# Optimization experiments

Measured on AMD Instinct MI355X. Metric: run time of the kernel, lower is better.

## Reference

```python
import jax, jax.numpy as jnp
import numpy as np

THRESHOLD = 0.5
NEG_POS_RATIO = 3
ALPHA = 1.0
B, P, C, O = 128, 8732, 21, 32


def xy_to_cxcy(xy):
    return jnp.concatenate([(xy[..., 2:] + xy[..., :2]) / 2, xy[..., 2:] - xy[..., :2]], axis=-1)


def cxcy_to_xy(cxcy):
    return jnp.concatenate([cxcy[..., :2] - cxcy[..., 2:] / 2, cxcy[..., :2] + cxcy[..., 2:] / 2], axis=-1)


def cxcy_to_gcxgcy(cxcy, priors_cxcy):
    g_cxcy = (cxcy[..., :2] - priors_cxcy[..., :2]) / (priors_cxcy[..., 2:] / 10.0)
    g_wh = jnp.log(cxcy[..., 2:] / priors_cxcy[..., 2:]) * 5.0
    return jnp.concatenate([g_cxcy, g_wh], axis=-1)


def find_jaccard_overlap(set1, set2):
    # set1: [O,4] xy, set2: [P,4] xy -> [O,P]
    lo = jnp.maximum(set1[:, None, :2], set2[None, :, :2])
    hi = jnp.minimum(set1[:, None, 2:], set2[None, :, 2:])
    inter = jnp.prod(jnp.clip(hi - lo, 0.0), axis=-1)
    a1 = jnp.prod(set1[:, 2:] - set1[:, :2], axis=-1)
    a2 = jnp.prod(set2[:, 2:] - set2[:, :2], axis=-1)
    union = a1[:, None] + a2[None, :] - inter
    return inter / union


def setup_inputs() -> dict:
    key = jax.random.key(0)
    k0, k1, k2, k3, k4, k5, k6 = jax.random.split(key, 7)
    predicted_locs = jax.random.normal(k0, (B, P, 4), jnp.float32)
    predicted_scores = jax.random.normal(k1, (B, P, C), jnp.float32)
    centers = jax.random.uniform(k2, (B, O, 2), jnp.float32, 0.2, 0.8)
    sizes = jax.random.uniform(k3, (B, O, 2), jnp.float32, 0.05, 0.3)
    boxes = jnp.concatenate([centers - sizes / 2, centers + sizes / 2], axis=-1)
    labels = jax.random.randint(k4, (B, O), 0, C)
    p_c = jax.random.uniform(k5, (P, 2), jnp.float32, 0.05, 0.95)
    p_wh = jax.random.uniform(k6, (P, 2), jnp.float32, 0.05, 0.5)
    priors_cxcy = jnp.concatenate([p_c, p_wh], axis=-1)
    return {"predicted_locs": predicted_locs, "predicted_scores": predicted_scores,
            "boxes": boxes, "labels": labels, "priors_cxcy": priors_cxcy}


def reference(predicted_locs, predicted_scores, boxes, labels, priors_cxcy):
    priors_xy = cxcy_to_xy(priors_cxcy)

    def match_one(boxes_i, labels_i):
        overlap = find_jaccard_overlap(boxes_i, priors_xy)           # [O,P]
        overlap_for_each_prior = jnp.max(overlap, axis=0)            # [P]
        object_for_each_prior = jnp.argmax(overlap, axis=0)          # [P]
        prior_for_each_object = jnp.argmax(overlap, axis=1)          # [O]
        object_for_each_prior = object_for_each_prior.at[prior_for_each_object].set(jnp.arange(O))
        overlap_for_each_prior = overlap_for_each_prior.at[prior_for_each_object].set(1.0)
        label_for_each_prior = labels_i[object_for_each_prior]
        label_for_each_prior = jnp.where(overlap_for_each_prior < THRESHOLD, 0, label_for_each_prior)
        true_locs_i = cxcy_to_gcxgcy(xy_to_cxcy(boxes_i[object_for_each_prior]), priors_cxcy)
        return label_for_each_prior, true_locs_i

    true_classes, true_locs = jax.vmap(match_one)(boxes, labels)     # [B,P], [B,P,4]

    positive = true_classes != 0                                     # [B,P]
    n_positives = jnp.sum(positive, axis=1)                          # [B]
    n_pos_total = jnp.sum(n_positives)

    # L1Loss (mean over selected positive elements, 4 per prior)
    abs_diff = jnp.abs(predicted_locs - true_locs)                   # [B,P,4]
    loc_loss = jnp.sum(abs_diff * positive[..., None]) / (n_pos_total.astype(jnp.float32) * 4.0)

    # per-element cross-entropy
    log_p = jax.nn.log_softmax(predicted_scores, axis=-1)            # [B,P,C]
    conf_loss_all = -jnp.take_along_axis(log_p, true_classes[..., None], axis=-1)[..., 0]  # [B,P]

    conf_loss_pos_sum = jnp.sum(jnp.where(positive, conf_loss_all, 0.0))
    conf_loss_neg = jnp.where(positive, 0.0, conf_loss_all)
    conf_loss_neg_sorted = -jnp.sort(-conf_loss_neg, axis=1)         # descending
    n_hard = NEG_POS_RATIO * n_positives                             # [B]
    hard_mask = jnp.arange(P)[None, :] < n_hard[:, None]             # [B,P]
    conf_loss_hard_neg_sum = jnp.sum(jnp.where(hard_mask, conf_loss_neg_sorted, 0.0))

    conf_loss = (conf_loss_hard_neg_sum + conf_loss_pos_sum) / n_pos_total.astype(jnp.float32)
    return conf_loss + ALPHA * loc_loss
```

## Files before the change

kernel.cpp:

```cpp
#include <hip/hip_runtime.h>
#include <hip/hip_bf16.h>

#define NB 128
#define NP 8732
#define NO 32
#define NC 21


__global__ __launch_bounds__(256) void k_init(int* ws) {
    int i = blockIdx.x * 256 + threadIdx.x;
    const int n = 36608 / 4;
    if (i < n) ws[i] = 0;
}

__device__ __forceinline__ float wave64_max_dpp(float m) {
    int v;
    v = __builtin_amdgcn_update_dpp(__float_as_int(m), __float_as_int(m), 0x111, 0xf, 0xf, false);
    m = fmaxf(m, __int_as_float(v));
    v = __builtin_amdgcn_update_dpp(__float_as_int(m), __float_as_int(m), 0x112, 0xf, 0xf, false);
    m = fmaxf(m, __int_as_float(v));
    v = __builtin_amdgcn_update_dpp(__float_as_int(m), __float_as_int(m), 0x114, 0xf, 0xf, false);
    m = fmaxf(m, __int_as_float(v));
    v = __builtin_amdgcn_update_dpp(__float_as_int(m), __float_as_int(m), 0x118, 0xf, 0xf, false);
    m = fmaxf(m, __int_as_float(v));
    v = __builtin_amdgcn_update_dpp(__float_as_int(m), __float_as_int(m), 0x142, 0xf, 0xf, false);
    m = fmaxf(m, __int_as_float(v));
    v = __builtin_amdgcn_update_dpp(__float_as_int(m), __float_as_int(m), 0x143, 0xf, 0xf, false);
    m = fmaxf(m, __int_as_float(v));
    return __int_as_float(__builtin_amdgcn_readlane(__float_as_int(m), 63));
}

__global__ __launch_bounds__(256) void k_match(const float* __restrict__ boxes,
                                               const float* __restrict__ priors,
                                               int* __restrict__ code,
                                               unsigned long long* __restrict__ packed) {
    int b = blockIdx.y;
    int tid = threadIdx.x;
    int base = blockIdx.x * 1024 + tid;
    int lane = tid & 63;

    __shared__ float4 sbox[NO];
    if (tid < NO)
        sbox[tid] = ((const float4*)(boxes + (size_t)b * NO * 4))[tid];
    __syncthreads();

    float px1[4], py1[4], px2[4], py2[4], pa[4];
    float bestv[4];
    int   besto[4];
#pragma unroll
    for (int j = 0; j < 4; ++j) {
        int p = base + 256 * j;
        int pp = p < NP ? p : NP - 1;
        float4 pr = ((const float4*)priors)[pp];
        px1[j] = pr.x - pr.z * 0.5f; py1[j] = pr.y - pr.w * 0.5f;
        px2[j] = pr.x + pr.z * 0.5f; py2[j] = pr.y + pr.w * 0.5f;
        pa[j]  = (px2[j] - px1[j]) * (py2[j] - py1[j]);
        bestv[j] = -1.0f; besto[j] = 0;
    }

    int wavep0 = blockIdx.x * 1024 + (tid & ~63);

#pragma unroll 2
    for (int o = 0; o < NO; ++o) {
        float4 bx = sbox[o];
        float a1 = (bx.z - bx.x) * (bx.w - bx.y);
        float iou[4];
#pragma unroll
        for (int j = 0; j < 4; ++j) {
            float lx = fmaxf(bx.x, px1[j]), ly = fmaxf(bx.y, py1[j]);
            float hx = fminf(bx.z, px2[j]), hy = fminf(bx.w, py2[j]);
            float iw = fmaxf(hx - lx, 0.0f), ih = fmaxf(hy - ly, 0.0f);
            float inter = iw * ih;
            iou[j] = inter / (a1 + pa[j] - inter);
            if (iou[j] > bestv[j]) { bestv[j] = iou[j]; besto[j] = o; }
        }
        float m = wave64_max_dpp(fmaxf(fmaxf(iou[0], iou[1]), fmaxf(iou[2], iou[3])));
        unsigned long long b0 = __ballot(iou[0] == m);
        unsigned long long b1 = __ballot(iou[1] == m);
        unsigned long long b2 = __ballot(iou[2] == m);
        unsigned long long b3 = __ballot(iou[3] == m);
        if (lane == 0) {
            unsigned long long bb; int jj;
            if (b0)      { bb = b0; jj = 0; }
            else if (b1) { bb = b1; jj = 1; }
            else if (b2) { bb = b2; jj = 2; }
            else         { bb = b3; jj = 3; }
            unsigned p = (unsigned)(wavep0 + 256 * jj) + (unsigned)(__ffsll(bb) - 1);
            unsigned long long key =
                ((unsigned long long)__float_as_uint(m) << 32) |
                (unsigned long long)(0xFFFFFFFFu - p);
            atomicMax(&packed[b * NO + o], key);
        }
    }
#pragma unroll
    for (int j = 0; j < 4; ++j) {
        int p = base + 256 * j;
        if (p < NP)
            code[(size_t)b * NP + p] = besto[j] | (bestv[j] >= 0.5f ? 256 : 0);
    }
}

__global__ __launch_bounds__(256) void k_loss(const float* __restrict__ plocs,
                                              const float* __restrict__ scores,
                                              const float* __restrict__ boxes,
                                              const int* __restrict__ labels,
                                              const float* __restrict__ priors,
                                              const int* __restrict__ code,
                                              const unsigned long long* __restrict__ packed,
                                              float* __restrict__ confneg,
                                              int* __restrict__ npos,
                                              double* __restrict__ accb) {
    __shared__ float srow[256 * NC];
    __shared__ unsigned spfl[NO];
    int b = blockIdx.y;
    int p0 = blockIdx.x * 256;
    int cnt = NP - p0; if (cnt > 256) cnt = 256;
    int nf4 = cnt * NC / 4;
    const float4* src4 = (const float4*)(scores + ((size_t)b * NP + p0) * NC);
    for (int i = threadIdx.x; i < nf4; i += 256)
        ((float4*)srow)[i] = src4[i];
    if (threadIdx.x < NO) {
        unsigned long long pk = packed[b * NO + threadIdx.x];
        spfl[threadIdx.x] = 0xFFFFFFFFu - (unsigned)(pk & 0xFFFFFFFFull);
    }
    __syncthreads();

    int p = p0 + threadIdx.x;
    float posconf = 0.0f, locpart = 0.0f;
    int isp = 0;

    if (p < NP) {
        int cd = code[(size_t)b * NP + p];
        int obj = cd & 255;
        int mat = cd >> 8;
#pragma unroll
        for (int o = 0; o < NO; ++o)
            if (spfl[o] == (unsigned)p) { obj = o; mat = 1; }
        int lbl = mat ? labels[b * NO + obj] : 0;

        const float* s = srow + threadIdx.x * NC;
        float m = s[0];
#pragma unroll
        for (int c = 1; c < NC; ++c) m = fmaxf(m, s[c]);
        float sum = 0.0f;
#pragma unroll
        for (int c = 0; c < NC; ++c) sum += __expf(s[c] - m);
        float conf = m + __logf(sum) - s[lbl];

        if (lbl != 0) {
            isp = 1;
            posconf = conf;
            float4 bx = ((const float4*)boxes)[b * NO + obj];
            float4 pr = ((const float4*)priors)[p];
            float cx = (bx.x + bx.z) * 0.5f, cy = (bx.y + bx.w) * 0.5f;
            float w = bx.z - bx.x, h = bx.w - bx.y;
            float gx = (cx - pr.x) / (pr.z * 0.1f);
            float gy = (cy - pr.y) / (pr.w * 0.1f);
            float gw = __logf(w / pr.z) * 5.0f;
            float gh = __logf(h / pr.w) * 5.0f;
            float4 pl = ((const float4*)plocs)[(size_t)b * NP + p];
            locpart = fabsf(pl.x - gx) + fabsf(pl.y - gy) +
                      fabsf(pl.z - gw) + fabsf(pl.w - gh);
        }
        confneg[(size_t)b * NP + p] = isp ? 0.0f : conf;
    }

    for (int s = 32; s > 0; s >>= 1) {
        posconf += __shfl_xor(posconf, s, 64);
        locpart += __shfl_xor(locpart, s, 64);
        isp     += __shfl_xor(isp, s, 64);
    }
    __shared__ float w0[4], w1[4];
    __shared__ int wc[4];
    int wid = threadIdx.x >> 6, lane = threadIdx.x & 63;
    if (lane == 0) { w0[wid] = posconf; w1[wid] = locpart; wc[wid] = isp; }
    __syncthreads();
    if (threadIdx.x == 0) {
        float t0 = w0[0] + w0[1] + w0[2] + w0[3];
        float t1 = w1[0] + w1[1] + w1[2] + w1[3];
        int   tc = wc[0] + wc[1] + wc[2] + wc[3];
        atomicAdd(&npos[b], tc);
        atomicAdd(&accb[b * 3 + 0], (double)t0);
        atomicAdd(&accb[b * 3 + 1], (double)t1);
    }
}

__global__ __launch_bounds__(1024) void k_topk(const float* __restrict__ confneg,
                                               const int* __restrict__ npos,
                                               double* __restrict__ accb,
                                               int* __restrict__ donecnt,
                                               float* __restrict__ out) {
    __shared__ int   si2[2][16];
    __shared__ int   si[16];
    __shared__ double sd[16];
    int tid = threadIdx.x, b = blockIdx.x;
    int lane = tid & 63, wid = tid >> 6;

    const float* src = confneg + (size_t)b * NP;
    float val[9];
#pragma unroll
    for (int j = 0; j < 9; ++j) {
        int i = tid + j * 1024;
        val[j] = (i < NP) ? src[i] : 0.0f;
    }
    int k = npos[b] * 3;
    if (k > NP) k = NP;

    if (k > 0) {
        unsigned T = 0;
        int par = 0;
        for (int bit = 30; bit >= 0; --bit) {
            unsigned cand = T | (1u << bit);
            int cnt = 0;
#pragma unroll
            for (int j = 0; j < 9; ++j)
                cnt += __popcll(__ballot(__float_as_uint(val[j]) >= cand));
            if (lane == 0) si2[par][wid] = cnt;
            __syncthreads();
            int t = 0;
#pragma unroll
            for (int w = 0; w < 16; ++w) t += si2[par][w];
            par ^= 1;
            if (t >= k) T = cand;
        }

        int cgt = 0;
        double sgt = 0.0;
#pragma unroll
        for (int j = 0; j < 9; ++j) {
            unsigned u = __float_as_uint(val[j]);
            if (u > T) { cgt++; sgt += (double)val[j]; }
        }
        for (int s = 32; s > 0; s >>= 1) {
            cgt += __shfl_xor(cgt, s, 64);
            sgt += __shfl_xor(sgt, s, 64);
        }
        if (lane == 0) { si[wid] = cgt; sd[wid] = sgt; }
        __syncthreads();
        if (tid == 0) {
            int cg = 0; double sg = 0.0;
            for (int w = 0; w < 16; ++w) { cg += si[w]; sg += sd[w]; }
            accb[b * 3 + 2] = sg + (double)(k - cg) * (double)__uint_as_float(T);
        }
    }

    __shared__ int samlast;
    if (tid == 0) {
        __threadfence();
        int prev = atomicAdd(donecnt, 1);
        samlast = (prev == NB - 1) ? 1 : 0;
    }
    __syncthreads();
    if (!samlast) return;
    __threadfence();

    double pc = 0.0, lc = 0.0, hn = 0.0, np_ = 0.0;
    if (tid < NB) {
        pc  = accb[tid * 3 + 0];
        lc  = accb[tid * 3 + 1];
        hn  = atomicAdd(&accb[tid * 3 + 2], 0.0);
        np_ = (double)npos[tid];
    }
    if (tid < 128) {
        for (int s = 32; s > 0; s >>= 1) {
            pc  += __shfl_xor(pc, s, 64);
            lc  += __shfl_xor(lc, s, 64);
            hn  += __shfl_xor(hn, s, 64);
            np_ += __shfl_xor(np_, s, 64);
        }
        if (lane == 0) { sd[wid * 4 + 0] = pc; sd[wid * 4 + 1] = lc;
                         sd[wid * 4 + 2] = hn; sd[wid * 4 + 3] = np_; }
    }
    __syncthreads();
    if (tid == 0) {
        double P = sd[0] + sd[4];
        double L = sd[1] + sd[5];
        double H = sd[2] + sd[6];
        double nt = sd[3] + sd[7];
        out[0] = (float)((H + P) / nt + L / (nt * 4.0));
    }
}

extern "C" void kernel_launch(void* const* d_in, const int* in_sizes, int n_in,
                              void* d_out, int out_size, void* d_ws, size_t ws_size,
                              hipStream_t stream) {
    const float* plocs  = (const float*)d_in[0];
    const float* scores = (const float*)d_in[1];
    const float* boxes  = (const float*)d_in[2];
    const int*   labels = (const int*)d_in[3];
    const float* priors = (const float*)d_in[4];
    float* out = (float*)d_out;

    char* ws = (char*)d_ws;
    unsigned long long* packed = (unsigned long long*)ws;
    int*    npos    = (int*)(ws + 32768);
    double* accb    = (double*)(ws + 33280);
    int*    donecnt = (int*)(ws + 36352);
    int*    code    = (int*)(ws + 36608);
    float*  confneg = (float*)(ws + 36608 + (size_t)NB * NP * 4);

    hipLaunchKernelGGL(k_init, dim3((36608 / 4 + 255) / 256), dim3(256), 0, stream, (int*)ws);
    hipLaunchKernelGGL(k_match, dim3((NP + 1023) / 1024, NB), dim3(256), 0, stream,
                       boxes, priors, code, packed);
    hipLaunchKernelGGL(k_loss, dim3((NP + 255) / 256, NB), dim3(256), 0, stream,
                       plocs, scores, boxes, labels, priors, code, packed, confneg, npos, accb);
    hipLaunchKernelGGL(k_topk, dim3(NB), dim3(1024), 0, stream, confneg, npos, accb, donecnt, out);
}
```

Baseline: 236.3 us.

## Split matching into atomic-free per-prior and per-object kernels, drop init kernel

Replaces the fused match kernel, which did wave reductions and 64-bit atomicMax per object, with two kernels: one computes the best object per prior, the other uses one wave per object to find that object's best prior. Per-block partial sums are written to buffers instead of double atomics, so the zero-init kernel can be removed. The top-k kernel now uses 256 threads with 35 values each and reduces the partials itself. The cost is IoU computed twice and one more launch, in exchange for removing atomics and the init launch.

```diff
diff --git a/kernel.cpp b/kernel.cpp
--- a/kernel.cpp
+++ b/kernel.cpp
@@ -5,15 +5,10 @@
 #define NP 8732
 #define NO 32
 #define NC 21
-
-
-__global__ __launch_bounds__(256) void k_init(int* ws) {
-    int i = blockIdx.x * 256 + threadIdx.x;
-    const int n = 36608 / 4;
-    if (i < n) ws[i] = 0;
-}
-
-__device__ __forceinline__ float wave64_max_dpp(float m) {
+#define NCHUNK 35
+
+
+__device__ __forceinline__ float wave64_fmax_u(float m) {
     int v;
     v = __builtin_amdgcn_update_dpp(__float_as_int(m), __float_as_int(m), 0x111, 0xf, 0xf, false);
     m = fmaxf(m, __int_as_float(v));
@@ -30,25 +25,34 @@
     return __int_as_float(__builtin_amdgcn_readlane(__float_as_int(m), 63));
 }
 
-__global__ __launch_bounds__(256) void k_match(const float* __restrict__ boxes,
-                                               const float* __restrict__ priors,
-                                               int* __restrict__ code,
-                                               unsigned long long* __restrict__ packed) {
+__device__ __forceinline__ int wave64_imin_u(int m) {
+    int v;
+    v = __builtin_amdgcn_update_dpp(m, m, 0x111, 0xf, 0xf, false); m = v < m ? v : m;
+    v = __builtin_amdgcn_update_dpp(m, m, 0x112, 0xf, 0xf, false); m = v < m ? v : m;
+    v = __builtin_amdgcn_update_dpp(m, m, 0x114, 0xf, 0xf, false); m = v < m ? v : m;
+    v = __builtin_amdgcn_update_dpp(m, m, 0x118, 0xf, 0xf, false); m = v < m ? v : m;
+    v = __builtin_amdgcn_update_dpp(m, m, 0x142, 0xf, 0xf, false); m = v < m ? v : m;
+    v = __builtin_amdgcn_update_dpp(m, m, 0x143, 0xf, 0xf, false); m = v < m ? v : m;
+    return __builtin_amdgcn_readlane(m, 63);
+}
+
+__global__ __launch_bounds__(256) void k_code(const float* __restrict__ boxes,
+                                              const float* __restrict__ priors,
+                                              int* __restrict__ code) {
     int b = blockIdx.y;
     int tid = threadIdx.x;
-    int base = blockIdx.x * 1024 + tid;
-    int lane = tid & 63;
+    int base = blockIdx.x * 512 + tid;
 
     __shared__ float4 sbox[NO];
     if (tid < NO)
         sbox[tid] = ((const float4*)(boxes + (size_t)b * NO * 4))[tid];
     __syncthreads();
 
-    float px1[4], py1[4], px2[4], py2[4], pa[4];
-    float bestv[4];
-    int   besto[4];
-#pragma unroll
-    for (int j = 0; j < 4; ++j) {
+    float px1[2], py1[2], px2[2], py2[2], pa[2];
+    float bestv[2];
+    int   besto[2];
+#pragma unroll
+    for (int j = 0; j < 2; ++j) {
         int p = base + 256 * j;
         int pp = p < NP ? p : NP - 1;
         float4 pr = ((const float4*)priors)[pp];
@@ -58,46 +62,70 @@
         bestv[j] = -1.0f; besto[j] = 0;
     }
 
-    int wavep0 = blockIdx.x * 1024 + (tid & ~63);
-
-#pragma unroll 2
+#pragma unroll
     for (int o = 0; o < NO; ++o) {
         float4 bx = sbox[o];
         float a1 = (bx.z - bx.x) * (bx.w - bx.y);
-        float iou[4];
-#pragma unroll
-        for (int j = 0; j < 4; ++j) {
+#pragma unroll
+        for (int j = 0; j < 2; ++j) {
             float lx = fmaxf(bx.x, px1[j]), ly = fmaxf(bx.y, py1[j]);
             float hx = fminf(bx.z, px2[j]), hy = fminf(bx.w, py2[j]);
             float iw = fmaxf(hx - lx, 0.0f), ih = fmaxf(hy - ly, 0.0f);
             float inter = iw * ih;
-            iou[j] = inter / (a1 + pa[j] - inter);
-            if (iou[j] > bestv[j]) { bestv[j] = iou[j]; besto[j] = o; }
-        }
-        float m = wave64_max_dpp(fmaxf(fmaxf(iou[0], iou[1]), fmaxf(iou[2], iou[3])));
-        unsigned long long b0 = __ballot(iou[0] == m);
-        unsigned long long b1 = __ballot(iou[1] == m);
-        unsigned long long b2 = __ballot(iou[2] == m);
-        unsigned long long b3 = __ballot(iou[3] == m);
-        if (lane == 0) {
-            unsigned long long bb; int jj;
-            if (b0)      { bb = b0; jj = 0; }
-            else if (b1) { bb = b1; jj = 1; }
-            else if (b2) { bb = b2; jj = 2; }
-            else         { bb = b3; jj = 3; }
-            unsigned p = (unsigned)(wavep0 + 256 * jj) + (unsigned)(__ffsll(bb) - 1);
-            unsigned long long key =
-                ((unsigned long long)__float_as_uint(m) << 32) |
-                (unsigned long long)(0xFFFFFFFFu - p);
-            atomicMax(&packed[b * NO + o], key);
-        }
-    }
-#pragma unroll
-    for (int j = 0; j < 4; ++j) {
+            float iou = inter / (a1 + pa[j] - inter);
+            if (iou > bestv[j]) { bestv[j] = iou; besto[j] = o; }
+        }
+    }
+#pragma unroll
+    for (int j = 0; j < 2; ++j) {
         int p = base + 256 * j;
         if (p < NP)
             code[(size_t)b * NP + p] = besto[j] | (bestv[j] >= 0.5f ? 256 : 0);
     }
+}
+
+__global__ __launch_bounds__(256) void k_obj(const float* __restrict__ boxes,
+                                             const float* __restrict__ priors,
+                                             int* __restrict__ pfor) {
+    int b = blockIdx.y;
+    int wid = threadIdx.x >> 6, lane = threadIdx.x & 63;
+    int o = blockIdx.x * 4 + wid;
+
+    float4 bx = ((const float4*)boxes)[b * NO + o];
+    float a1 = (bx.z - bx.x) * (bx.w - bx.y);
+    const float4* pr4 = (const float4*)priors;
+
+    float bv = -1.0f; int bp = 0;
+    for (int i = 0; i < 136; ++i) {
+        int p = lane + (i << 6);
+        float4 pr = pr4[p];
+        float x1 = pr.x - pr.z * 0.5f, y1 = pr.y - pr.w * 0.5f;
+        float x2 = pr.x + pr.z * 0.5f, y2 = pr.y + pr.w * 0.5f;
+        float pa = (x2 - x1) * (y2 - y1);
+        float lx = fmaxf(bx.x, x1), ly = fmaxf(bx.y, y1);
+        float hx = fminf(bx.z, x2), hy = fminf(bx.w, y2);
+        float inter = fmaxf(hx - lx, 0.0f) * fmaxf(hy - ly, 0.0f);
+        float iou = inter / (a1 + pa - inter);
+        if (iou > bv) { bv = iou; bp = p; }
+    }
+    {
+        int p = lane + 8704;
+        if (p < NP) {
+            float4 pr = pr4[p];
+            float x1 = pr.x - pr.z * 0.5f, y1 = pr.y - pr.w * 0.5f;
+            float x2 = pr.x + pr.z * 0.5f, y2 = pr.y + pr.w * 0.5f;
+            float pa = (x2 - x1) * (y2 - y1);
+            float lx = fmaxf(bx.x, x1), ly = fmaxf(bx.y, y1);
+            float hx = fminf(bx.z, x2), hy = fminf(bx.w, y2);
+            float inter = fmaxf(hx - lx, 0.0f) * fmaxf(hy - ly, 0.0f);
+            float iou = inter / (a1 + pa - inter);
+            if (iou > bv) { bv = iou; bp = p; }
+        }
+    }
+    float m = wave64_fmax_u(bv);
+    int pc = (bv == m) ? bp : 0x7FFFFFFF;
+    int mp = wave64_imin_u(pc);
+    if (lane == 0) pfor[b * NO + o] = mp;
 }
 
 __global__ __launch_bounds__(256) void k_loss(const float* __restrict__ plocs,
@@ -106,12 +134,14 @@
                                               const int* __restrict__ labels,
                                               const float* __restrict__ priors,
                                               const int* __restrict__ code,
-                                              const unsigned long long* __restrict__ packed,
+                                              const int* __restrict__ pfor,
                                               float* __restrict__ confneg,
-                                              int* __restrict__ npos,
-                                              double* __restrict__ accb) {
+                                              int* __restrict__ pnp,
+                                              double* __restrict__ pd0,
+                                              double* __restrict__ pd1,
+                                              int* __restrict__ donecnt) {
     __shared__ float srow[256 * NC];
-    __shared__ unsigned spfl[NO];
+    __shared__ int spfl[NO];
     int b = blockIdx.y;
     int p0 = blockIdx.x * 256;
     int cnt = NP - p0; if (cnt > 256) cnt = 256;
@@ -119,10 +149,8 @@
     const float4* src4 = (const float4*)(scores + ((size_t)b * NP + p0) * NC);
     for (int i = threadIdx.x; i < nf4; i += 256)
         ((float4*)srow)[i] = src4[i];
-    if (threadIdx.x < NO) {
-        unsigned long long pk = packed[b * NO + threadIdx.x];
-        spfl[threadIdx.x] = 0xFFFFFFFFu - (unsigned)(pk & 0xFFFFFFFFull);
-    }
+    if (threadIdx.x < NO)
+        spfl[threadIdx.x] = pfor[b * NO + threadIdx.x];
     __syncthreads();
 
     int p = p0 + threadIdx.x;
@@ -135,7 +163,7 @@
         int mat = cd >> 8;
 #pragma unroll
         for (int o = 0; o < NO; ++o)
-            if (spfl[o] == (unsigned)p) { obj = o; mat = 1; }
+            if (spfl[o] == p) { obj = o; mat = 1; }
         int lbl = mat ? labels[b * NO + obj] : 0;
 
         const float* s = srow + threadIdx.x * NC;
@@ -176,36 +204,60 @@
     if (lane == 0) { w0[wid] = posconf; w1[wid] = locpart; wc[wid] = isp; }
     __syncthreads();
     if (threadIdx.x == 0) {
-        float t0 = w0[0] + w0[1] + w0[2] + w0[3];
-        float t1 = w1[0] + w1[1] + w1[2] + w1[3];
-        int   tc = wc[0] + wc[1] + wc[2] + wc[3];
-        atomicAdd(&npos[b], tc);
-        atomicAdd(&accb[b * 3 + 0], (double)t0);
-        atomicAdd(&accb[b * 3 + 1], (double)t1);
-    }
-}
-
-__global__ __launch_bounds__(1024) void k_topk(const float* __restrict__ confneg,
-                                               const int* __restrict__ npos,
-                                               double* __restrict__ accb,
-                                               int* __restrict__ donecnt,
-                                               float* __restrict__ out) {
-    __shared__ int   si2[2][16];
-    __shared__ int   si[16];
-    __shared__ double sd[16];
+        int pb = b * NCHUNK + blockIdx.x;
+        pd0[pb] = (double)(w0[0] + w0[1] + w0[2] + w0[3]);
+        pd1[pb] = (double)(w1[0] + w1[1] + w1[2] + w1[3]);
+        pnp[pb] = wc[0] + wc[1] + wc[2] + wc[3];
+        if (pb == 0) *donecnt = 0;
+    }
+}
+
+__global__ __launch_bounds__(256) void k_topk(const float* __restrict__ confneg,
+                                              const int* __restrict__ pnp,
+                                              const double* __restrict__ pd0,
+                                              const double* __restrict__ pd1,
+                                              int* __restrict__ snp,
+                                              double* __restrict__ sums,
+                                              int* __restrict__ donecnt,
+                                              float* __restrict__ out) {
+    __shared__ int    si2[2][4];
+    __shared__ int    siw[4];
+    __shared__ double sdd[4];
+    __shared__ int    sk;
     int tid = threadIdx.x, b = blockIdx.x;
     int lane = tid & 63, wid = tid >> 6;
 
+    if (wid == 0) {
+        int np_ = 0; double d0 = 0.0, d1 = 0.0;
+        if (lane < NCHUNK) {
+            int pb = b * NCHUNK + lane;
+            np_ = pnp[pb]; d0 = pd0[pb]; d1 = pd1[pb];
+        }
+        for (int s = 32; s > 0; s >>= 1) {
+            np_ += __shfl_xor(np_, s, 64);
+            d0  += __shfl_xor(d0, s, 64);
+            d1  += __shfl_xor(d1, s, 64);
+        }
+        if (lane == 0) {
+            int k = np_ * 3; if (k > NP) k = NP;
+            sk = k;
+            snp[b] = np_;
+            sums[b * 3 + 1] = d0;
+            sums[b * 3 + 2] = d1;
+        }
+    }
+
     const float* src = confneg + (size_t)b * NP;
-    float val[9];
-#pragma unroll
-    for (int j = 0; j < 9; ++j) {
-        int i = tid + j * 1024;
+    float val[35];
+#pragma unroll
+    for (int j = 0; j < 35; ++j) {
+        int i = tid + j * 256;
         val[j] = (i < NP) ? src[i] : 0.0f;
     }
-    int k = npos[b] * 3;
-    if (k > NP) k = NP;
-
+    __syncthreads();
+    int k = sk;
+
+    double hn = 0.0;
     if (k > 0) {
         unsigned T = 0;
         int par = 0;
@@ -213,13 +265,11 @@
             unsigned cand = T | (1u << bit);
             int cnt = 0;
 #pragma unroll
-            for (int j = 0; j < 9; ++j)
+            for (int j = 0; j < 35; ++j)
                 cnt += __popcll(__ballot(__float_as_uint(val[j]) >= cand));
             if (lane == 0) si2[par][wid] = cnt;
             __syncthreads();
-            int t = 0;
-#pragma unroll
-            for (int w = 0; w < 16; ++w) t += si2[par][w];
+            int t = si2[par][0] + si2[par][1] + si2[par][2] + si2[par][3];
             par ^= 1;
             if (t >= k) T = cand;
         }
@@ -227,7 +277,7 @@
         int cgt = 0;
         double sgt = 0.0;
 #pragma unroll
-        for (int j = 0; j < 9; ++j) {
+        for (int j = 0; j < 35; ++j) {
             unsigned u = __float_as_uint(val[j]);
             if (u > T) { cgt++; sgt += (double)val[j]; }
         }
@@ -235,14 +285,15 @@
             cgt += __shfl_xor(cgt, s, 64);
             sgt += __shfl_xor(sgt, s, 64);
         }
-        if (lane == 0) { si[wid] = cgt; sd[wid] = sgt; }
+        if (lane == 0) { siw[wid] = cgt; sdd[wid] = sgt; }
         __syncthreads();
         if (tid == 0) {
-            int cg = 0; double sg = 0.0;
-            for (int w = 0; w < 16; ++w) { cg += si[w]; sg += sd[w]; }
-            accb[b * 3 + 2] = sg + (double)(k - cg) * (double)__uint_as_float(T);
-        }
-    }
+            int cg = siw[0] + siw[1] + siw[2] + siw[3];
+            double sg = sdd[0] + sdd[1] + sdd[2] + sdd[3];
+            hn = sg + (double)(k - cg) * (double)__uint_as_float(T);
+        }
+    }
+    if (tid == 0) sums[b * 3 + 0] = hn;
 
     __shared__ int samlast;
     if (tid == 0) {
@@ -254,29 +305,29 @@
     if (!samlast) return;
     __threadfence();
 
-    double pc = 0.0, lc = 0.0, hn = 0.0, np_ = 0.0;
+    double hnn = 0.0, pc = 0.0, lc = 0.0, npd = 0.0;
     if (tid < NB) {
-        pc  = accb[tid * 3 + 0];
-        lc  = accb[tid * 3 + 1];
-        hn  = atomicAdd(&accb[tid * 3 + 2], 0.0);
-        np_ = (double)npos[tid];
-    }
-    if (tid < 128) {
-        for (int s = 32; s > 0; s >>= 1) {
-            pc  += __shfl_xor(pc, s, 64);
-            lc  += __shfl_xor(lc, s, 64);
-            hn  += __shfl_xor(hn, s, 64);
-            np_ += __shfl_xor(np_, s, 64);
-        }
-        if (lane == 0) { sd[wid * 4 + 0] = pc; sd[wid * 4 + 1] = lc;
-                         sd[wid * 4 + 2] = hn; sd[wid * 4 + 3] = np_; }
+        hnn = atomicAdd(&sums[tid * 3 + 0], 0.0);
+        pc  = atomicAdd(&sums[tid * 3 + 1], 0.0);
+        lc  = atomicAdd(&sums[tid * 3 + 2], 0.0);
+        npd = (double)atomicAdd((int*)&snp[tid], 0);
+    }
+    for (int s = 32; s > 0; s >>= 1) {
+        hnn += __shfl_xor(hnn, s, 64);
+        pc  += __shfl_xor(pc, s, 64);
+        lc  += __shfl_xor(lc, s, 64);
+        npd += __shfl_xor(npd, s, 64);
+    }
+    __shared__ double sfin[4][2];
+    if (lane == 0 && wid < 2) {
+        sfin[0][wid] = hnn; sfin[1][wid] = pc; sfin[2][wid] = lc; sfin[3][wid] = npd;
     }
     __syncthreads();
     if (tid == 0) {
-        double P = sd[0] + sd[4];
-        double L = sd[1] + sd[5];
-        double H = sd[2] + sd[6];
-        double nt = sd[3] + sd[7];
+        double H  = sfin[0][0] + sfin[0][1];
+        double P  = sfin[1][0] + sfin[1][1];
+        double L  = sfin[2][0] + sfin[2][1];
+        double nt = sfin[3][0] + sfin[3][1];
         out[0] = (float)((H + P) / nt + L / (nt * 4.0));
     }
 }
@@ -292,17 +343,23 @@
     float* out = (float*)d_out;
 
     char* ws = (char*)d_ws;
-    unsigned long long* packed = (unsigned long long*)ws;
-    int*    npos    = (int*)(ws + 32768);
-    double* accb    = (double*)(ws + 33280);
-    int*    donecnt = (int*)(ws + 36352);
-    int*    code    = (int*)(ws + 36608);
-    float*  confneg = (float*)(ws + 36608 + (size_t)NB * NP * 4);
-
-    hipLaunchKernelGGL(k_init, dim3((36608 / 4 + 255) / 256), dim3(256), 0, stream, (int*)ws);
-    hipLaunchKernelGGL(k_match, dim3((NP + 1023) / 1024, NB), dim3(256), 0, stream,
-                       boxes, priors, code, packed);
-    hipLaunchKernelGGL(k_loss, dim3((NP + 255) / 256, NB), dim3(256), 0, stream,
-                       plocs, scores, boxes, labels, priors, code, packed, confneg, npos, accb);
-    hipLaunchKernelGGL(k_topk, dim3(NB), dim3(1024), 0, stream, confneg, npos, accb, donecnt, out);
-}
+    int*    pfor    = (int*)ws;
+    double* pd0     = (double*)(ws + 16384);
+    double* pd1     = (double*)(ws + 52224);
+    int*    pnp     = (int*)(ws + 88064);
+    int*    snp     = (int*)(ws + 105984);
+    double* sums    = (double*)(ws + 106496);
+    int*    donecnt = (int*)(ws + 109568);
+    int*    code    = (int*)(ws + 109824);
+    float*  confneg = (float*)(ws + 4580608);
+
+    hipLaunchKernelGGL(k_code, dim3((NP + 511) / 512, NB), dim3(256), 0, stream,
+                       boxes, priors, code);
+    hipLaunchKernelGGL(k_obj, dim3(NO / 4, NB), dim3(256), 0, stream,
+                       boxes, priors, pfor);
+    hipLaunchKernelGGL(k_loss, dim3(NCHUNK, NB), dim3(256), 0, stream,
+                       plocs, scores, boxes, labels, priors, code, pfor,
+                       confneg, pnp, pd0, pd1, donecnt);
+    hipLaunchKernelGGL(k_topk, dim3(NB), dim3(256), 0, stream,
+                       confneg, pnp, pd0, pd1, snp, sums, donecnt, out);
+}
```

Result: no change. 240.1 us (+1.6%).
